# Optimization experiments

Measured on AMD Instinct MI355X. Metric: run time of the kernel, lower is better.

The kernel has to match this reference:

```python
import jax, jax.numpy as jnp
import numpy as np

N = 50000        # nodes
E = 800000       # edges
IN_FEAT = 128
OUT_FEAT = 64
HEADS = 4
NUM_CLASSES = 40
NEG_SLOPE = 0.2  # DGL GATConv default


def setup_inputs() -> dict:
    key = jax.random.key(0)
    ks = jax.random.split(key, 12)
    x = jax.random.normal(ks[0], (N, IN_FEAT), dtype=jnp.float32)
    src = jax.random.randint(ks[1], (E,), 0, N, dtype=jnp.int32)
    dst = jax.random.randint(ks[2], (E,), 0, N, dtype=jnp.int32)
    # layer 1 params: fc W1 [in, H*D], attn_l/attn_r [H, D], bias [H*D]
    s1 = 1.0 / np.sqrt(IN_FEAT)
    W1 = jax.random.normal(ks[3], (IN_FEAT, HEADS * OUT_FEAT), dtype=jnp.float32) * s1
    al1 = jax.random.normal(ks[4], (HEADS, OUT_FEAT), dtype=jnp.float32) * 0.1
    ar1 = jax.random.normal(ks[5], (HEADS, OUT_FEAT), dtype=jnp.float32) * 0.1
    b1 = jnp.zeros((HEADS * OUT_FEAT,), dtype=jnp.float32)
    # layer 2 params: fc W2 [H*D, C], attn [1, C], bias [C]
    hid = HEADS * OUT_FEAT
    s2 = 1.0 / np.sqrt(hid)
    W2 = jax.random.normal(ks[6], (hid, NUM_CLASSES), dtype=jnp.float32) * s2
    al2 = jax.random.normal(ks[7], (1, NUM_CLASSES), dtype=jnp.float32) * 0.1
    ar2 = jax.random.normal(ks[8], (1, NUM_CLASSES), dtype=jnp.float32) * 0.1
    b2 = jnp.zeros((NUM_CLASSES,), dtype=jnp.float32)
    return {"x": x, "src": src, "dst": dst,
            "W1": W1, "al1": al1, "ar1": ar1, "b1": b1,
            "W2": W2, "al2": al2, "ar2": ar2, "b2": b2}


def gat_layer(x, W, al, ar, bias, src, dst, heads, out_feat):
    n = x.shape[0]
    h = (x @ W).reshape(n, heads, out_feat)            # [N,H,D]
    el = jnp.sum(h * al[None], axis=-1)                # [N,H]
    er = jnp.sum(h * ar[None], axis=-1)                # [N,H]
    e = el[src] + er[dst]                              # [E,H]
    e = jnp.where(e > 0, e, NEG_SLOPE * e)             # LeakyReLU
    # segment softmax over edges sharing the same destination
    emax = jax.ops.segment_max(e, dst, num_segments=n)           # [N,H]
    emax = jnp.where(jnp.isfinite(emax), emax, 0.0)              # isolated nodes
    ee = jnp.exp(e - emax[dst])                                  # [E,H]
    denom = jax.ops.segment_sum(ee, dst, num_segments=n)         # [N,H]
    denom = jnp.where(denom > 0, denom, 1.0)
    alpha = ee / denom[dst]                                      # [E,H]
    msg = h[src] * alpha[:, :, None]                             # [E,H,D]
    out = jax.ops.segment_sum(msg, dst, num_segments=n)          # [N,H,D]
    return out + bias.reshape(1, heads, out_feat)


def reference(x, src, dst, W1, al1, ar1, b1, W2, al2, ar2, b2):
    h = gat_layer(x, W1, al1, ar1, b1, src, dst, HEADS, OUT_FEAT)  # [N,H,D]
    h = h.reshape(h.shape[0], HEADS * OUT_FEAT)
    h = jax.nn.elu(h)
    h = gat_layer(h, W2, al2, ar2, b2, src, dst, 1, NUM_CLASSES)   # [N,1,C]
    return jnp.squeeze(h, axis=1)                                   # [N,C]
```

## Files before the change

kernel.cpp:

```cpp
#include <hip/hip_runtime.h>

#define NN 50000
#define NE 800000
#define HID 256
#define NCLS 40

typedef short bf16x8 __attribute__((ext_vector_type(8)));
typedef float f32x4 __attribute__((ext_vector_type(4)));

__device__ inline unsigned short f2bf(float f) {
    unsigned int u = __float_as_uint(f);
    return (unsigned short)((u + 0x7FFFu + ((u >> 16) & 1u)) >> 16);
}
__device__ inline unsigned int pack2bf(float a, float b) {
    return (unsigned int)f2bf(a) | ((unsigned int)f2bf(b) << 16);
}
__device__ inline float2 bf2x(unsigned int u) {
    return make_float2(__uint_as_float(u << 16), __uint_as_float(u & 0xFFFF0000u));
}

__global__ void k_scanA(const int* __restrict__ counts, int* __restrict__ indptr,
                        int* __restrict__ bsum) {
    __shared__ int sh[256];
    int t = threadIdx.x;
    int idx = blockIdx.x * 256 + t;
    int c = idx < NN ? counts[idx] : 0;
    sh[t] = c;
    __syncthreads();
    for (int off = 1; off < 256; off <<= 1) {
        int v = (t >= off) ? sh[t - off] : 0;
        __syncthreads();
        sh[t] += v;
        __syncthreads();
    }
    if (idx < NN) indptr[idx] = sh[t] - c;
    if (t == 255) bsum[blockIdx.x] = sh[255];
}

__global__ void k_scanB(int* __restrict__ bsum, int nb) {
    __shared__ int sh[256];
    int t = threadIdx.x;
    int c = t < nb ? bsum[t] : 0;
    sh[t] = c;
    __syncthreads();
    for (int off = 1; off < 256; off <<= 1) {
        int v = (t >= off) ? sh[t - off] : 0;
        __syncthreads();
        sh[t] += v;
        __syncthreads();
    }
    if (t < nb) bsum[t] = sh[t] - c;
}

__global__ void k_scanC(int* __restrict__ indptr, const int* __restrict__ bsum,
                        int* __restrict__ fill) {
    int idx = blockIdx.x * 256 + threadIdx.x;
    if (idx < NN) {
        indptr[idx] += bsum[idx >> 8];
        fill[idx] = 0;
    }
    if (idx == 0) indptr[NN] = NE;
}

__global__ void k_scatterw(const int* __restrict__ src, const int* __restrict__ dst,
                           const int* __restrict__ indptr, int* __restrict__ fill,
                           const float* __restrict__ el1, const float* __restrict__ er1,
                           int* __restrict__ srcs, float4* __restrict__ w4) {
    int e = blockIdx.x * 256 + threadIdx.x;
    if (e < NE) {
        int d = dst[e];
        int s = src[e];
        int pos = atomicAdd(&fill[d], 1);
        int j = indptr[d] + pos;
        srcs[j] = s;
        float4 ls = *(const float4*)&el1[(size_t)s * 4];
        float4 rd = *(const float4*)&er1[(size_t)d * 4];
        float e0 = ls.x + rd.x, e1 = ls.y + rd.y, e2 = ls.z + rd.z, e3 = ls.w + rd.w;
        e0 = e0 > 0.f ? e0 : 0.2f * e0;
        e1 = e1 > 0.f ? e1 : 0.2f * e1;
        e2 = e2 > 0.f ? e2 : 0.2f * e2;
        e3 = e3 > 0.f ? e3 : 0.2f * e3;
        w4[j] = make_float4(__expf(e0), __expf(e1), __expf(e2), __expf(e3));
    }
}

__global__ void k_prep(const float* __restrict__ W1, const float* __restrict__ al,
                       const float* __restrict__ ar, const float* __restrict__ W2,
                       float* __restrict__ wel, float* __restrict__ wer,
                       unsigned short* __restrict__ W1Tb,
                       unsigned short* __restrict__ W2Tb) {
    int gid = blockIdx.x * 256 + threadIdx.x;
    int nth = gridDim.x * 256;
    const int TOT = 512 + 32768 + 48 * 256;
    for (int i = gid; i < TOT; i += nth) {
        if (i < 512) {
            int k = i >> 2, h = i & 3;
            float a = 0.f, b = 0.f;
            for (int dd = 0; dd < 64; ++dd) {
                float w = W1[k * 256 + h * 64 + dd];
                a = fmaf(w, al[h * 64 + dd], a);
                b = fmaf(w, ar[h * 64 + dd], b);
            }
            wel[i] = a;
            wer[i] = b;
        } else if (i < 512 + 32768) {
            int j = i - 512;
            int col = j >> 7, k = j & 127;
            W1Tb[j] = f2bf(W1[k * 256 + col]);
        } else {
            int j = i - 512 - 32768;
            int col = j >> 8, kk = j & 255;
            W2Tb[j] = (col < NCLS) ? f2bf(W2[kk * 40 + col]) : (unsigned short)0;
        }
    }
}

__global__ void k_elr1x(const float* __restrict__ x, const float* __restrict__ wel,
                        const float* __restrict__ wer, float* __restrict__ el1,
                        float* __restrict__ er1, unsigned short* __restrict__ xb,
                        const int* __restrict__ dst, int* __restrict__ counts) {
    __shared__ float xs[64 * 129];
    __shared__ float wels[512], wers[512];
    int t = threadIdx.x;
    int n0 = blockIdx.x * 64;
    wels[t] = wel[t]; wels[256 + t] = wel[256 + t];
    wers[t] = wer[t]; wers[256 + t] = wer[256 + t];
    for (int i = 0; i < 8; ++i) {
        int f = i * 256 + t;
        int row = f >> 5;
        int col4 = (f & 31) * 4;
        float4 v = make_float4(0.f, 0.f, 0.f, 0.f);
        if (n0 + row < NN) v = ((const float4*)x)[(size_t)n0 * 32 + f];
        xs[row * 129 + col4 + 0] = v.x;
        xs[row * 129 + col4 + 1] = v.y;
        xs[row * 129 + col4 + 2] = v.z;
        xs[row * 129 + col4 + 3] = v.w;
    }
    __syncthreads();
    int node = t & 63;
    int h = t >> 6;
    float a = 0.f, b = 0.f;
    for (int k = 0; k < 128; ++k) {
        float xv = xs[node * 129 + k];
        a = fmaf(xv, wels[k * 4 + h], a);
        b = fmaf(xv, wers[k * 4 + h], b);
    }
    if (n0 + node < NN) {
        el1[(size_t)(n0 + node) * 4 + h] = a;
        er1[(size_t)(n0 + node) * 4 + h] = b;
    }
    for (int i = 0; i < 4; ++i) {
        int g = (i * 256 + t) * 8;
        int row = g >> 7, col = g & 127;
        if (n0 + row < NN) {
            ushort4 lo, hi;
            lo.x = f2bf(xs[row * 129 + col + 0]);
            lo.y = f2bf(xs[row * 129 + col + 1]);
            lo.z = f2bf(xs[row * 129 + col + 2]);
            lo.w = f2bf(xs[row * 129 + col + 3]);
            hi.x = f2bf(xs[row * 129 + col + 4]);
            hi.y = f2bf(xs[row * 129 + col + 5]);
            hi.z = f2bf(xs[row * 129 + col + 6]);
            hi.w = f2bf(xs[row * 129 + col + 7]);
            *(ushort4*)&xb[(size_t)(n0 + row) * 128 + col] = lo;
            *(ushort4*)&xb[(size_t)(n0 + row) * 128 + col + 4] = hi;
        }
    }
    int gid = blockIdx.x * 256 + t;
    int nth = gridDim.x * 256;
    for (int e = gid; e < NE; e += nth) atomicAdd(&counts[dst[e]], 1);
}

#define XG_STRIDE 260
#define EB_STRIDE 264
#define FMA8(AC0, AC1, AC2, AC3, WQ, XV) \
    AC0.x = fmaf(WQ.x, XV.x, AC0.x); AC0.y = fmaf(WQ.x, XV.y, AC0.y); \
    AC1.x = fmaf(WQ.y, XV.x, AC1.x); AC1.y = fmaf(WQ.y, XV.y, AC1.y); \
    AC2.x = fmaf(WQ.z, XV.x, AC2.x); AC2.y = fmaf(WQ.z, XV.y, AC2.y); \
    AC3.x = fmaf(WQ.w, XV.x, AC3.x); AC3.y = fmaf(WQ.w, XV.y, AC3.y);

__global__ void k_agg1m(const unsigned int* __restrict__ xb32,
                        const float4* __restrict__ w4,
                        const int* __restrict__ indptr, const int* __restrict__ srcs,
                        const unsigned short* __restrict__ W1Tb,
                        const unsigned short* __restrict__ W2Tb,
                        const float* __restrict__ b1,
                        const float* __restrict__ al2, const float* __restrict__ ar2,
                        unsigned short* __restrict__ h2b,
                        float* __restrict__ el2, float* __restrict__ er2) {
    __shared__ unsigned int xg[16 * XG_STRIDE];
    __shared__ __align__(16) unsigned char pool[10496];
    float4 (*sw)[64] = (float4(*)[64])pool;
    int (*si)[64] = (int(*)[64])(pool + 8192);
    unsigned short* eb = (unsigned short*)pool;
    float* pel = (float*)(pool + 8448);
    float* per_ = (float*)(pool + 8640);
    int t = threadIdx.x;
    int wv = t >> 6, l = t & 63;
    int n0 = blockIdx.x * 16;
    int d0 = n0 + wv * 4;
    int ip[5];
#pragma unroll
    for (int q = 0; q < 5; ++q) ip[q] = indptr[d0 + q];
    int w2 = wv * 2;
#pragma unroll
    for (int p = 0; p < 2; ++p) {
        int begA = ip[2 * p + 0], endA = ip[2 * p + 1];
        int begB = ip[2 * p + 1], endB = ip[2 * p + 2];
        int degA = endA - begA, degB = endB - begB;
        int sA = 0, sB = 0;
        float4 wA = make_float4(0.f, 0.f, 0.f, 0.f);
        float4 wB = make_float4(0.f, 0.f, 0.f, 0.f);
        if (l < degA) { sA = srcs[begA + l]; wA = w4[begA + l]; }
        if (l < degB) { sB = srcs[begB + l]; wB = w4[begB + l]; }
        si[w2 + 0][l] = sA; sw[w2 + 0][l] = wA;
        si[w2 + 1][l] = sB; sw[w2 + 1][l] = wB;
        float2 aA0 = {0,0}, aA1 = {0,0}, aA2 = {0,0}, aA3 = {0,0};
        float2 aB0 = {0,0}, aB1 = {0,0}, aB2 = {0,0}, aB3 = {0,0};
        int capA = degA < 64 ? degA : 64;
        int capB = degB < 64 ? degB : 64;
        int mcap = capA > capB ? capA : capB;
        for (int e = 0; e < mcap; e += 8) {
            unsigned int uA[8], uB[8];
            bool doA = e < capA, doB = e < capB;
            if (doA) {
#pragma unroll
                for (int q = 0; q < 8; ++q)
                    uA[q] = xb32[(size_t)si[w2][e + q] * 64 + l];
            }
            if (doB) {
#pragma unroll
                for (int q = 0; q < 8; ++q)
                    uB[q] = xb32[(size_t)si[w2 + 1][e + q] * 64 + l];
            }
            if (doA) {
#pragma unroll
                for (int q = 0; q < 8; ++q) {
                    float4 wq = sw[w2][e + q];
                    float2 xv = bf2x(uA[q]);
                    FMA8(aA0, aA1, aA2, aA3, wq, xv)
                }
            }
            if (doB) {
#pragma unroll
                for (int q = 0; q < 8; ++q) {
                    float4 wq = sw[w2 + 1][e + q];
                    float2 xv = bf2x(uB[q]);
                    FMA8(aB0, aB1, aB2, aB3, wq, xv)
                }
            }
        }
        for (int j = begA + 64; j < endA; ++j) {
            float4 wq = w4[j];
            float2 xv = bf2x(xb32[(size_t)srcs[j] * 64 + l]);
            FMA8(aA0, aA1, aA2, aA3, wq, xv)
        }
        for (int j = begB + 64; j < endB; ++j) {
            float4 wq = w4[j];
            float2 xv = bf2x(xb32[(size_t)srcs[j] * 64 + l]);
            FMA8(aB0, aB1, aB2, aB3, wq, xv)
        }
        float dA0 = wA.x, dA1 = wA.y, dA2 = wA.z, dA3 = wA.w;
        float dB0 = wB.x, dB1 = wB.y, dB2 = wB.z, dB3 = wB.w;
        for (int j = begA + 64 + l; j < endA; j += 64) {
            float4 wt = w4[j];
            dA0 += wt.x; dA1 += wt.y; dA2 += wt.z; dA3 += wt.w;
        }
        for (int j = begB + 64 + l; j < endB; j += 64) {
            float4 wt = w4[j];
            dB0 += wt.x; dB1 += wt.y; dB2 += wt.z; dB3 += wt.w;
        }
#pragma unroll
        for (int off = 32; off > 0; off >>= 1) {
            dA0 += __shfl_xor(dA0, off); dA1 += __shfl_xor(dA1, off);
            dA2 += __shfl_xor(dA2, off); dA3 += __shfl_xor(dA3, off);
            dB0 += __shfl_xor(dB0, off); dB1 += __shfl_xor(dB1, off);
            dB2 += __shfl_xor(dB2, off); dB3 += __shfl_xor(dB3, off);
        }
        float iA0 = dA0 > 0.f ? 1.f / dA0 : 0.f;
        float iA1 = dA1 > 0.f ? 1.f / dA1 : 0.f;
        float iA2 = dA2 > 0.f ? 1.f / dA2 : 0.f;
        float iA3 = dA3 > 0.f ? 1.f / dA3 : 0.f;
        float iB0 = dB0 > 0.f ? 1.f / dB0 : 0.f;
        float iB1 = dB1 > 0.f ? 1.f / dB1 : 0.f;
        float iB2 = dB2 > 0.f ? 1.f / dB2 : 0.f;
        float iB3 = dB3 > 0.f ? 1.f / dB3 : 0.f;
        unsigned int* xgA = &xg[(wv * 4 + 2 * p + 0) * XG_STRIDE];
        xgA[0 * 64 + l] = pack2bf(aA0.x * iA0, aA0.y * iA0);
        xgA[1 * 64 + l] = pack2bf(aA1.x * iA1, aA1.y * iA1);
        xgA[2 * 64 + l] = pack2bf(aA2.x * iA2, aA2.y * iA2);
        xgA[3 * 64 + l] = pack2bf(aA3.x * iA3, aA3.y * iA3);
        unsigned int* xgB = &xg[(wv * 4 + 2 * p + 1) * XG_STRIDE];
        xgB[0 * 64 + l] = pack2bf(aB0.x * iB0, aB0.y * iB0);
        xgB[1 * 64 + l] = pack2bf(aB1.x * iB1, aB1.y * iB1);
        xgB[2 * 64 + l] = pack2bf(aB2.x * iB2, aB2.y * iB2);
        xgB[3 * 64 + l] = pack2bf(aB3.x * iB3, aB3.y * iB3);
    }
    __syncthreads();
    int lrow = l & 15, lk = l >> 4;
    {
        f32x4 acc[4] = {};
#pragma unroll
        for (int kt = 0; kt < 4; ++kt) {
            bf16x8 av = *(const bf16x8*)&xg[lrow * XG_STRIDE + wv * 64 + kt * 16 + lk * 4];
#pragma unroll
            for (int nt = 0; nt < 4; ++nt) {
                int col = wv * 64 + nt * 16 + lrow;
                bf16x8 bv = *(const bf16x8*)&W1Tb[(size_t)col * 128 + kt * 32 + lk * 8];
                acc[nt] = __builtin_amdgcn_mfma_f32_16x16x32_bf16(av, bv, acc[nt], 0, 0, 0);
            }
        }
#pragma unroll
        for (int nt = 0; nt < 4; ++nt) {
            int col = wv * 64 + nt * 16 + lrow;
            float bv1 = b1[col];
#pragma unroll
            for (int r = 0; r < 4; ++r) {
                int rloc = lk * 4 + r;
                float o = acc[nt][r] + bv1;
                o = o > 0.f ? o : (__expf(o) - 1.f);
                eb[rloc * EB_STRIDE + col] = f2bf(o);
            }
        }
    }
    __syncthreads();
    if (wv < 3) {
        f32x4 acc2 = {};
#pragma unroll
        for (int kt = 0; kt < 8; ++kt) {
            bf16x8 av = *(const bf16x8*)&eb[lrow * EB_STRIDE + kt * 32 + lk * 8];
            bf16x8 bv = *(const bf16x8*)&W2Tb[(size_t)(wv * 16 + lrow) * 256 + kt * 32 + lk * 8];
            acc2 = __builtin_amdgcn_mfma_f32_16x16x32_bf16(av, bv, acc2, 0, 0, 0);
        }
        int col2 = wv * 16 + lrow;
        float alc = col2 < NCLS ? al2[col2] : 0.f;
        float arc = col2 < NCLS ? ar2[col2] : 0.f;
#pragma unroll
        for (int r = 0; r < 4; ++r) {
            int row = n0 + lk * 4 + r;
            float v = acc2[r];
            if (col2 < NCLS) h2b[(size_t)row * NCLS + col2] = f2bf(v);
            float pa = v * alc, pb = v * arc;
#pragma unroll
            for (int off = 1; off < 16; off <<= 1) {
                pa += __shfl_xor(pa, off);
                pb += __shfl_xor(pb, off);
            }
            if (lrow == 0) {
                pel[wv * 16 + lk * 4 + r] = pa;
                per_[wv * 16 + lk * 4 + r] = pb;
            }
        }
    }
    __syncthreads();
    if (t < 16) {
        el2[n0 + t] = pel[t] + pel[16 + t] + pel[32 + t];
        er2[n0 + t] = per_[t] + per_[16 + t] + per_[32 + t];
    }
}

__global__ void k_agg2(const unsigned int* __restrict__ h2b32,
                       const float* __restrict__ el2,
                       const float* __restrict__ er2, const float* __restrict__ b2,
                       const int* __restrict__ indptr, const int* __restrict__ srcs,
                       float* __restrict__ out) {
    __shared__ int   si[8][64];
    __shared__ float sw[8][64];
    int t = threadIdx.x;
    int wv = t >> 6, l = t & 63;
    int dA = blockIdx.x * 8 + wv * 2;
    int dB = dA + 1;
    int begA = indptr[dA], endA = indptr[dA + 1];
    int begB = endA, endB = indptr[dB + 1];
    int degA = endA - begA, degB = endB - begB;
    float rdA = er2[dA], rdB = er2[dB];
    int sA = 0, sB = 0;
    float wA = 0.f, wB = 0.f;
    if (l < degA) {
        sA = srcs[begA + l];
        float e = el2[sA] + rdA;
        e = e > 0.f ? e : 0.2f * e;
        wA = __expf(e);
    }
    if (l < degB) {
        sB = srcs[begB + l];
        float e = el2[sB] + rdB;
        e = e > 0.f ? e : 0.2f * e;
        wB = __expf(e);
    }
    int w2 = wv * 2;
    si[w2 + 0][l] = sA; sw[w2 + 0][l] = wA;
    si[w2 + 1][l] = sB; sw[w2 + 1][l] = wB;
    float denA = wA, denB = wB;
    for (int j = begA + 64 + l; j < endA; j += 64) {
        float e = el2[srcs[j]] + rdA;
        e = e > 0.f ? e : 0.2f * e;
        denA += __expf(e);
    }
    for (int j = begB + 64 + l; j < endB; j += 64) {
        float e = el2[srcs[j]] + rdB;
        e = e > 0.f ? e : 0.2f * e;
        denB += __expf(e);
    }
    int half = l >> 5, il = l & 31;
    bool act = il < 20;
    float2 accA = {0.f, 0.f}, accB = {0.f, 0.f};
    int capA = degA < 64 ? degA : 64;
    int capB = degB < 64 ? degB : 64;
    int mcap = capA > capB ? capA : capB;
    for (int e = 0; e < mcap; e += 8) {
        bool doA = e < capA, doB = e < capB;
        int ixA[4], ixB[4];
        float wsA[4], wsB[4];
        unsigned int uA[4], uB[4];
        if (doA) {
#pragma unroll
            for (int q = 0; q < 4; ++q) {
                int idx = e + 2 * q + half;
                ixA[q] = si[w2][idx];
                wsA[q] = sw[w2][idx];
            }
        }
        if (doB) {
#pragma unroll
            for (int q = 0; q < 4; ++q) {
                int idx = e + 2 * q + half;
                ixB[q] = si[w2 + 1][idx];
                wsB[q] = sw[w2 + 1][idx];
            }
        }
        if (doA) {
#pragma unroll
            for (int q = 0; q < 4; ++q)
                uA[q] = act ? h2b32[(size_t)ixA[q] * 20 + il] : 0u;
        }
        if (doB) {
#pragma unroll
            for (int q = 0; q < 4; ++q)
                uB[q] = act ? h2b32[(size_t)ixB[q] * 20 + il] : 0u;
        }
        if (doA) {
#pragma unroll
            for (int q = 0; q < 4; ++q) {
                float2 xv = bf2x(uA[q]);
                accA.x = fmaf(wsA[q], xv.x, accA.x);
                accA.y = fmaf(wsA[q], xv.y, accA.y);
            }
        }
        if (doB) {
#pragma unroll
            for (int q = 0; q < 4; ++q) {
                float2 xv = bf2x(uB[q]);
                accB.x = fmaf(wsB[q], xv.x, accB.x);
                accB.y = fmaf(wsB[q], xv.y, accB.y);
            }
        }
    }
    for (int j = begA + 64; j < endA; ++j) {
        int s = srcs[j];
        float e = el2[s] + rdA;
        e = e > 0.f ? e : 0.2f * e;
        float ww = (half == 0) ? __expf(e) : 0.f;
        unsigned int u = act ? h2b32[(size_t)s * 20 + il] : 0u;
        float2 xv = bf2x(u);
        accA.x = fmaf(ww, xv.x, accA.x);
        accA.y = fmaf(ww, xv.y, accA.y);
    }
    for (int j = begB + 64; j < endB; ++j) {
        int s = srcs[j];
        float e = el2[s] + rdB;
        e = e > 0.f ? e : 0.2f * e;
        float ww = (half == 0) ? __expf(e) : 0.f;
        unsigned int u = act ? h2b32[(size_t)s * 20 + il] : 0u;
        float2 xv = bf2x(u);
        accB.x = fmaf(ww, xv.x, accB.x);
        accB.y = fmaf(ww, xv.y, accB.y);
    }
#pragma unroll
    for (int off = 32; off > 0; off >>= 1) {
        denA += __shfl_xor(denA, off);
        denB += __shfl_xor(denB, off);
    }
    float invA = denA > 0.f ? 1.f / denA : 0.f;
    float invB = denB > 0.f ? 1.f / denB : 0.f;
    accA.x += __shfl_xor(accA.x, 32);
    accA.y += __shfl_xor(accA.y, 32);
    accB.x += __shfl_xor(accB.x, 32);
    accB.y += __shfl_xor(accB.y, 32);
    if (half == 0 && act) {
        float2 bb = *(const float2*)&b2[2 * il];
        *(float2*)&out[(size_t)dA * NCLS + 2 * il] =
            make_float2(fmaf(accA.x, invA, bb.x), fmaf(accA.y, invA, bb.y));
        *(float2*)&out[(size_t)dB * NCLS + 2 * il] =
            make_float2(fmaf(accB.x, invB, bb.x), fmaf(accB.y, invB, bb.y));
    }
}

extern "C" void kernel_launch(void* const* d_in, const int* in_sizes, int n_in,
                              void* d_out, int out_size, void* d_ws, size_t ws_size,
                              hipStream_t stream) {
    const float* x   = (const float*)d_in[0];
    const int*   src = (const int*)d_in[1];
    const int*   dst = (const int*)d_in[2];
    const float* W1  = (const float*)d_in[3];
    const float* al1 = (const float*)d_in[4];
    const float* ar1 = (const float*)d_in[5];
    const float* b1  = (const float*)d_in[6];
    const float* W2  = (const float*)d_in[7];
    const float* al2 = (const float*)d_in[8];
    const float* ar2 = (const float*)d_in[9];
    const float* b2  = (const float*)d_in[10];
    float* out = (float*)d_out;

    float* ws = (float*)d_ws;
    size_t off = 0;
    unsigned short* xb    = (unsigned short*)(ws + off); off += (size_t)NN * 64;
    unsigned short* h2b   = (unsigned short*)(ws + off); off += (size_t)NN * 20;
    float* el1  = ws + off; off += (size_t)NN * 4;
    float* er1  = ws + off; off += (size_t)NN * 4;
    float* el2  = ws + off; off += NN;
    float* er2  = ws + off; off += NN;
    float* wel  = ws + off; off += 512;
    float* wer  = ws + off; off += 512;
    unsigned short* w1tb = (unsigned short*)(ws + off); off += 16384;
    unsigned short* w2tb = (unsigned short*)(ws + off); off += 48 * 128;
    float* w4   = ws + off; off += (size_t)NE * 4;
    int* counts = (int*)(ws + off);
    int* indptr = counts + NN;
    int* fill   = indptr + NN + 1;
    int* srcs   = fill + NN;
    int* bsum   = srcs + NE;

    const int NB = (NN + 255) / 256;

    hipMemsetAsync(counts, 0, NN * sizeof(int), stream);

    k_prep<<<48, 256, 0, stream>>>(W1, al1, ar1, W2, wel, wer, w1tb, w2tb);
    k_elr1x<<<(NN + 63) / 64, 256, 0, stream>>>(x, wel, wer, el1, er1, xb, dst, counts);
    k_scanA<<<NB, 256, 0, stream>>>(counts, indptr, bsum);
    k_scanB<<<1, 256, 0, stream>>>(bsum, NB);
    k_scanC<<<NB, 256, 0, stream>>>(indptr, bsum, fill);
    k_scatterw<<<(NE + 255) / 256, 256, 0, stream>>>(src, dst, indptr, fill,
                                                     el1, er1, srcs, (float4*)w4);
    k_agg1m<<<NN / 16, 256, 0, stream>>>((const unsigned int*)xb, (const float4*)w4,
                                         indptr, srcs, w1tb, w2tb, b1, al2, ar2,
                                         h2b, el2, er2);

    k_agg2<<<NN / 8, 256, 0, stream>>>((const unsigned int*)h2b, el2, er2, b2,
                                       indptr, srcs, out);
}
```

Baseline: 202.5 us.

## Split layer-1 aggregation from MFMA projection and quarter-split gather across blocks

Splits the fused gather+MFMA kernel into two kernels. The aggregation kernel now spreads each node tile over four blocks: each block handles a 16-word column slice, and lanes split edges into four groups that are combined with cross-lane shuffles. The aggregated features go to a new global bf16 buffer, which a separate MFMA kernel reads to do the W1 projection and the layer-2 prep. This is meant to raise parallelism and memory-level concurrency in the gather, at the cost of an extra global write and read of the aggregated features, an extra launch, and a fourfold re-read of the per-node srcs/w4 lists.

Measured after the change: 281.5 us. 39.0% more time.

```diff
diff --git a/kernel.cpp b/kernel.cpp
--- a/kernel.cpp
+++ b/kernel.cpp
@@ -171,37 +171,29 @@
     for (int e = gid; e < NE; e += nth) atomicAdd(&counts[dst[e]], 1);
 }
 
-#define XG_STRIDE 260
-#define EB_STRIDE 264
-#define FMA8(AC0, AC1, AC2, AC3, WQ, XV) \
-    AC0.x = fmaf(WQ.x, XV.x, AC0.x); AC0.y = fmaf(WQ.x, XV.y, AC0.y); \
-    AC1.x = fmaf(WQ.y, XV.x, AC1.x); AC1.y = fmaf(WQ.y, XV.y, AC1.y); \
-    AC2.x = fmaf(WQ.z, XV.x, AC2.x); AC2.y = fmaf(WQ.z, XV.y, AC2.y); \
-    AC3.x = fmaf(WQ.w, XV.x, AC3.x); AC3.y = fmaf(WQ.w, XV.y, AC3.y);
-
-__global__ void k_agg1m(const unsigned int* __restrict__ xb32,
-                        const float4* __restrict__ w4,
-                        const int* __restrict__ indptr, const int* __restrict__ srcs,
-                        const unsigned short* __restrict__ W1Tb,
-                        const unsigned short* __restrict__ W2Tb,
-                        const float* __restrict__ b1,
-                        const float* __restrict__ al2, const float* __restrict__ ar2,
-                        unsigned short* __restrict__ h2b,
-                        float* __restrict__ el2, float* __restrict__ er2) {
-    __shared__ unsigned int xg[16 * XG_STRIDE];
-    __shared__ __align__(16) unsigned char pool[10496];
-    float4 (*sw)[64] = (float4(*)[64])pool;
-    int (*si)[64] = (int(*)[64])(pool + 8192);
-    unsigned short* eb = (unsigned short*)pool;
-    float* pel = (float*)(pool + 8448);
-    float* per_ = (float*)(pool + 8640);
+#define EFMA8(H0, H1, H2, H3, WQ, XV) \
+    H0.x = fmaf(WQ.x, XV.x, H0.x); H0.y = fmaf(WQ.x, XV.y, H0.y); \
+    H1.x = fmaf(WQ.y, XV.x, H1.x); H1.y = fmaf(WQ.y, XV.y, H1.y); \
+    H2.x = fmaf(WQ.z, XV.x, H2.x); H2.y = fmaf(WQ.z, XV.y, H2.y); \
+    H3.x = fmaf(WQ.w, XV.x, H3.x); H3.y = fmaf(WQ.w, XV.y, H3.y);
+
+__global__ void k_aggQ(const unsigned int* __restrict__ xb32,
+                       const float4* __restrict__ w4,
+                       const int* __restrict__ indptr, const int* __restrict__ srcs,
+                       unsigned int* __restrict__ xaggb) {
+    __shared__ int   si[8][64];
+    __shared__ float4 sw[8][64];
     int t = threadIdx.x;
     int wv = t >> 6, l = t & 63;
-    int n0 = blockIdx.x * 16;
+    int q = blockIdx.x & 3;
+    int tile = blockIdx.x >> 2;
+    int u = l & 15, g = l >> 4;
+    int qbase = q * 16 + u;
+    int n0 = tile * 16;
     int d0 = n0 + wv * 4;
     int ip[5];
 #pragma unroll
-    for (int q = 0; q < 5; ++q) ip[q] = indptr[d0 + q];
+    for (int k = 0; k < 5; ++k) ip[k] = indptr[d0 + k];
     int w2 = wv * 2;
 #pragma unroll
     for (int p = 0; p < 2; ++p) {
@@ -215,50 +207,48 @@
         if (l < degB) { sB = srcs[begB + l]; wB = w4[begB + l]; }
         si[w2 + 0][l] = sA; sw[w2 + 0][l] = wA;
         si[w2 + 1][l] = sB; sw[w2 + 1][l] = wB;
-        float2 aA0 = {0,0}, aA1 = {0,0}, aA2 = {0,0}, aA3 = {0,0};
-        float2 aB0 = {0,0}, aB1 = {0,0}, aB2 = {0,0}, aB3 = {0,0};
+        float2 hA0 = {0,0}, hA1 = {0,0}, hA2 = {0,0}, hA3 = {0,0};
+        float2 hB0 = {0,0}, hB1 = {0,0}, hB2 = {0,0}, hB3 = {0,0};
         int capA = degA < 64 ? degA : 64;
         int capB = degB < 64 ? degB : 64;
         int mcap = capA > capB ? capA : capB;
         for (int e = 0; e < mcap; e += 8) {
-            unsigned int uA[8], uB[8];
             bool doA = e < capA, doB = e < capB;
+            int i0A = 0, i1A = 0, i0B = 0, i1B = 0;
+            float4 w0A, w1A, w0B, w1B;
+            unsigned int u0A = 0, u1A = 0, u0B = 0, u1B = 0;
             if (doA) {
-#pragma unroll
-                for (int q = 0; q < 8; ++q)
-                    uA[q] = xb32[(size_t)si[w2][e + q] * 64 + l];
+                i0A = si[w2][e + g];     w0A = sw[w2][e + g];
+                i1A = si[w2][e + 4 + g]; w1A = sw[w2][e + 4 + g];
+                u0A = xb32[(size_t)i0A * 64 + qbase];
+                u1A = xb32[(size_t)i1A * 64 + qbase];
             }
             if (doB) {
-#pragma unroll
-                for (int q = 0; q < 8; ++q)
-                    uB[q] = xb32[(size_t)si[w2 + 1][e + q] * 64 + l];
+                i0B = si[w2 + 1][e + g];     w0B = sw[w2 + 1][e + g];
+                i1B = si[w2 + 1][e + 4 + g]; w1B = sw[w2 + 1][e + 4 + g];
+                u0B = xb32[(size_t)i0B * 64 + qbase];
+                u1B = xb32[(size_t)i1B * 64 + qbase];
             }
             if (doA) {
-#pragma unroll
-                for (int q = 0; q < 8; ++q) {
-                    float4 wq = sw[w2][e + q];
-                    float2 xv = bf2x(uA[q]);
-                    FMA8(aA0, aA1, aA2, aA3, wq, xv)
-                }
+                float2 x0 = bf2x(u0A), x1 = bf2x(u1A);
+                EFMA8(hA0, hA1, hA2, hA3, w0A, x0)
+                EFMA8(hA0, hA1, hA2, hA3, w1A, x1)
             }
             if (doB) {
-#pragma unroll
-                for (int q = 0; q < 8; ++q) {
-                    float4 wq = sw[w2 + 1][e + q];
-                    float2 xv = bf2x(uB[q]);
-                    FMA8(aB0, aB1, aB2, aB3, wq, xv)
-                }
-            }
-        }
-        for (int j = begA + 64; j < endA; ++j) {
+                float2 x0 = bf2x(u0B), x1 = bf2x(u1B);
+                EFMA8(hB0, hB1, hB2, hB3, w0B, x0)
+                EFMA8(hB0, hB1, hB2, hB3, w1B, x1)
+            }
+        }
+        for (int j = begA + 64 + g; j < endA; j += 4) {
             float4 wq = w4[j];
-            float2 xv = bf2x(xb32[(size_t)srcs[j] * 64 + l]);
-            FMA8(aA0, aA1, aA2, aA3, wq, xv)
-        }
-        for (int j = begB + 64; j < endB; ++j) {
+            float2 xv = bf2x(xb32[(size_t)srcs[j] * 64 + qbase]);
+            EFMA8(hA0, hA1, hA2, hA3, wq, xv)
+        }
+        for (int j = begB + 64 + g; j < endB; j += 4) {
             float4 wq = w4[j];
-            float2 xv = bf2x(xb32[(size_t)srcs[j] * 64 + l]);
-            FMA8(aB0, aB1, aB2, aB3, wq, xv)
+            float2 xv = bf2x(xb32[(size_t)srcs[j] * 64 + qbase]);
+            EFMA8(hB0, hB1, hB2, hB3, wq, xv)
         }
         float dA0 = wA.x, dA1 = wA.y, dA2 = wA.z, dA3 = wA.w;
         float dB0 = wB.x, dB1 = wB.y, dB2 = wB.z, dB3 = wB.w;
@@ -285,24 +275,48 @@
         float iB1 = dB1 > 0.f ? 1.f / dB1 : 0.f;
         float iB2 = dB2 > 0.f ? 1.f / dB2 : 0.f;
         float iB3 = dB3 > 0.f ? 1.f / dB3 : 0.f;
-        unsigned int* xgA = &xg[(wv * 4 + 2 * p + 0) * XG_STRIDE];
-        xgA[0 * 64 + l] = pack2bf(aA0.x * iA0, aA0.y * iA0);
-        xgA[1 * 64 + l] = pack2bf(aA1.x * iA1, aA1.y * iA1);
-        xgA[2 * 64 + l] = pack2bf(aA2.x * iA2, aA2.y * iA2);
-        xgA[3 * 64 + l] = pack2bf(aA3.x * iA3, aA3.y * iA3);
-        unsigned int* xgB = &xg[(wv * 4 + 2 * p + 1) * XG_STRIDE];
-        xgB[0 * 64 + l] = pack2bf(aB0.x * iB0, aB0.y * iB0);
-        xgB[1 * 64 + l] = pack2bf(aB1.x * iB1, aB1.y * iB1);
-        xgB[2 * 64 + l] = pack2bf(aB2.x * iB2, aB2.y * iB2);
-        xgB[3 * 64 + l] = pack2bf(aB3.x * iB3, aB3.y * iB3);
-    }
-    __syncthreads();
+#pragma unroll
+        for (int off = 16; off <= 32; off <<= 1) {
+            hA0.x += __shfl_xor(hA0.x, off); hA0.y += __shfl_xor(hA0.y, off);
+            hA1.x += __shfl_xor(hA1.x, off); hA1.y += __shfl_xor(hA1.y, off);
+            hA2.x += __shfl_xor(hA2.x, off); hA2.y += __shfl_xor(hA2.y, off);
+            hA3.x += __shfl_xor(hA3.x, off); hA3.y += __shfl_xor(hA3.y, off);
+            hB0.x += __shfl_xor(hB0.x, off); hB0.y += __shfl_xor(hB0.y, off);
+            hB1.x += __shfl_xor(hB1.x, off); hB1.y += __shfl_xor(hB1.y, off);
+            hB2.x += __shfl_xor(hB2.x, off); hB2.y += __shfl_xor(hB2.y, off);
+            hB3.x += __shfl_xor(hB3.x, off); hB3.y += __shfl_xor(hB3.y, off);
+        }
+        float2 vA = g == 0 ? hA0 : (g == 1 ? hA1 : (g == 2 ? hA2 : hA3));
+        float  jA = g == 0 ? iA0 : (g == 1 ? iA1 : (g == 2 ? iA2 : iA3));
+        float2 vB = g == 0 ? hB0 : (g == 1 ? hB1 : (g == 2 ? hB2 : hB3));
+        float  jB = g == 0 ? iB0 : (g == 1 ? iB1 : (g == 2 ? iB2 : iB3));
+        int dA_ = d0 + 2 * p, dB_ = dA_ + 1;
+        xaggb[(size_t)dA_ * 256 + g * 64 + qbase] = pack2bf(vA.x * jA, vA.y * jA);
+        xaggb[(size_t)dB_ * 256 + g * 64 + qbase] = pack2bf(vB.x * jB, vB.y * jB);
+    }
+}
+
+#define EB_STRIDE 264
+__global__ void k_mfma12(const unsigned short* __restrict__ xaggb,
+                         const unsigned short* __restrict__ W1Tb,
+                         const unsigned short* __restrict__ W2Tb,
+                         const float* __restrict__ b1,
+                         const float* __restrict__ al2, const float* __restrict__ ar2,
+                         unsigned short* __restrict__ h2b,
+                         float* __restrict__ el2, float* __restrict__ er2) {
+    __shared__ __align__(16) unsigned char pool[8832];
+    unsigned short* eb = (unsigned short*)pool;
+    float* pel = (float*)(pool + 8448);
+    float* per_ = (float*)(pool + 8640);
+    int t = threadIdx.x;
+    int wv = t >> 6, l = t & 63;
+    int n0 = blockIdx.x * 16;
     int lrow = l & 15, lk = l >> 4;
     {
         f32x4 acc[4] = {};
 #pragma unroll
         for (int kt = 0; kt < 4; ++kt) {
-            bf16x8 av = *(const bf16x8*)&xg[lrow * XG_STRIDE + wv * 64 + kt * 16 + lk * 4];
+            bf16x8 av = *(const bf16x8*)&xaggb[((size_t)(n0 + lrow) * 4 + wv) * 128 + kt * 32 + lk * 8];
 #pragma unroll
             for (int nt = 0; nt < 4; ++nt) {
                 int col = wv * 64 + nt * 16 + lrow;
@@ -516,6 +530,7 @@
     size_t off = 0;
     unsigned short* xb    = (unsigned short*)(ws + off); off += (size_t)NN * 64;
     unsigned short* h2b   = (unsigned short*)(ws + off); off += (size_t)NN * 20;
+    unsigned int*   xaggb = (unsigned int*)(ws + off);   off += (size_t)NN * 256;
     float* el1  = ws + off; off += (size_t)NN * 4;
     float* er1  = ws + off; off += (size_t)NN * 4;
     float* el2  = ws + off; off += NN;
@@ -542,9 +557,10 @@
     k_scanC<<<NB, 256, 0, stream>>>(indptr, bsum, fill);
     k_scatterw<<<(NE + 255) / 256, 256, 0, stream>>>(src, dst, indptr, fill,
                                                      el1, er1, srcs, (float4*)w4);
-    k_agg1m<<<NN / 16, 256, 0, stream>>>((const unsigned int*)xb, (const float4*)w4,
-                                         indptr, srcs, w1tb, w2tb, b1, al2, ar2,
-                                         h2b, el2, er2);
+    k_aggQ<<<(NN / 16) * 4, 256, 0, stream>>>((const unsigned int*)xb, (const float4*)w4,
+                                              indptr, srcs, xaggb);
+    k_mfma12<<<NN / 16, 256, 0, stream>>>((const unsigned short*)xaggb, w1tb, w2tb,
+                                          b1, al2, ar2, h2b, el2, er2);
 
     k_agg2<<<NN / 8, 256, 0, stream>>>((const unsigned int*)h2b, el2, er2, b2,
                                        indptr, srcs, out);
```
